# Kernel optimization log

Measured on AMD Instinct MI355X. Metric: run time of the kernel, lower is better.

Reference implementation:

```python
import jax, jax.numpy as jnp
import numpy as np

CENTER_RADIUS = 2.5
TOPK = 13
IOU_WEIGHT = 3.0
BETA = 2.0
NUM_CLASSES = 80
BBOX_W = 2.0
BIG = 1e8
EPS = 1e-7
IMG = 1280


def pairwise_iou(boxes, gts):
    # boxes [N,4], gts [M,4] xyxy -> [N,M]
    lt = jnp.maximum(boxes[:, None, :2], gts[None, :, :2])
    rb = jnp.minimum(boxes[:, None, 2:], gts[None, :, 2:])
    wh = jnp.clip(rb - lt, 0.0)
    inter = wh[..., 0] * wh[..., 1]
    area_a = (boxes[:, 2] - boxes[:, 0]) * (boxes[:, 3] - boxes[:, 1])
    area_b = (gts[:, 2] - gts[:, 0]) * (gts[:, 3] - gts[:, 1])
    union = area_a[:, None] + area_b[None, :] - inter
    return inter / jnp.maximum(union, EPS)


def giou_elementwise(a, b):
    # a,b [N,4] xyxy -> [N]
    lt = jnp.maximum(a[:, :2], b[:, :2])
    rb = jnp.minimum(a[:, 2:], b[:, 2:])
    wh = jnp.clip(rb - lt, 0.0)
    inter = wh[:, 0] * wh[:, 1]
    area_a = (a[:, 2] - a[:, 0]) * (a[:, 3] - a[:, 1])
    area_b = (b[:, 2] - b[:, 0]) * (b[:, 3] - b[:, 1])
    union = area_a + area_b - inter
    iou = inter / jnp.maximum(union, EPS)
    elt = jnp.minimum(a[:, :2], b[:, :2])
    erb = jnp.maximum(a[:, 2:], b[:, 2:])
    ewh = jnp.clip(erb - elt, 0.0)
    enclose = ewh[:, 0] * ewh[:, 1]
    return iou - (enclose - union) / jnp.maximum(enclose, EPS)


def simota_assign(pred_scores, pred_boxes, points, strides, gt_boxes, gt_labels):
    N = points.shape[0]
    M = gt_boxes.shape[0]
    px, py = points[:, 0], points[:, 1]
    # Step 1: candidate selection (inside box OR inside center region)
    in_box = ((px[:, None] > gt_boxes[None, :, 0]) & (py[:, None] > gt_boxes[None, :, 1]) &
              (px[:, None] < gt_boxes[None, :, 2]) & (py[:, None] < gt_boxes[None, :, 3]))
    gcx = (gt_boxes[:, 0] + gt_boxes[:, 2]) * 0.5
    gcy = (gt_boxes[:, 1] + gt_boxes[:, 3]) * 0.5
    r = CENTER_RADIUS * strides[:, None]
    in_center = ((px[:, None] > gcx[None, :] - r) & (py[:, None] > gcy[None, :] - r) &
                 (px[:, None] < gcx[None, :] + r) & (py[:, None] < gcy[None, :] + r))
    is_cand = in_box | in_center          # [N,M]
    cand_any = is_cand.any(axis=1)        # [N]
    # Step 2: cost = BCE(prob, onehot) + w * (-log IoU)
    iou = pairwise_iou(pred_boxes, gt_boxes)  # [N,M]
    p = jnp.clip(pred_scores, 1e-6, 1.0 - 1e-6)
    log_p = jnp.log(p)
    log_1mp = jnp.log1p(-p)
    all_neg = -log_1mp.sum(axis=-1)       # [N] sum_c BCE(p_c, 0)
    cls_cost = all_neg[:, None] + log_1mp[:, gt_labels] - log_p[:, gt_labels]
    reg_cost = -jnp.log(iou + EPS)
    cost = cls_cost + IOU_WEIGHT * reg_cost
    cost = jnp.where(is_cand, cost, BIG)
    # Step 3: dynamic k from top-k IoUs over candidate points (candidates of any gt)
    iou_cand = jnp.where(cand_any[:, None], iou, 0.0)
    topk_ious, _ = jax.lax.top_k(iou_cand.T, TOPK)            # [M,TOPK]
    dyn_k = jnp.clip(topk_ious.sum(axis=-1).astype(jnp.int32), 1, None)  # [M], <= TOPK
    # Step 4: per-gt lowest-cost candidates; k_j entries, only valid (cost < BIG)
    neg_top, top_idx = jax.lax.top_k(-cost.T, TOPK)           # [M,TOPK]
    top_cost = -neg_top
    ranks = jnp.arange(TOPK)
    select = (ranks[None, :] < dyn_k[:, None]) & (top_cost < BIG)
    matching = jnp.zeros((N, M), bool).at[top_idx, jnp.arange(M)[:, None]].set(select)
    # Step 5: conflict resolution -> keep lowest-cost gt per point
    matched = matching.any(axis=1)
    best = jnp.argmin(jnp.where(matching, cost, jnp.inf), axis=1)  # [N]
    rows = jnp.arange(N)
    labels = jnp.where(matched, gt_labels[best], NUM_CLASSES)
    aboxes = jnp.where(matched[:, None], gt_boxes[best], 0.0)
    pos_iou = jnp.where(matched, iou[rows, best], 0.0)
    ascores = jnp.zeros((N, NUM_CLASSES), pred_scores.dtype).at[rows, gt_labels[best]].set(pos_iou)
    return labels, aboxes, ascores


def reference(pred_logits, pred_boxes, points, strides, gt_boxes, gt_labels):
    pred_scores = jax.nn.sigmoid(pred_logits)
    sg = jax.lax.stop_gradient
    labels, aboxes, ascores = simota_assign(sg(pred_scores), sg(pred_boxes),
                                            sg(points), sg(strides), sg(gt_boxes), gt_labels)
    labels, aboxes, ascores = sg(labels), sg(aboxes), sg(ascores)
    # Quality Focal Loss
    x, t = pred_logits, ascores
    bce = jnp.maximum(x, 0.0) - x * t + jnp.log1p(jnp.exp(-jnp.abs(x)))
    scale = jnp.abs(t - pred_scores) ** BETA
    n_pos_cls = jnp.maximum(1, (t > 0).sum()).astype(x.dtype)
    loss_cls = (scale * bce).sum() / n_pos_cls
    # GIoU loss over positives
    matched = labels < NUM_CLASSES
    g = giou_elementwise(pred_boxes, aboxes)
    n_pos = jnp.maximum(1, matched.sum()).astype(x.dtype)
    loss_box = jnp.where(matched, 1.0 - g, 0.0).sum() / n_pos
    return loss_cls + BBOX_W * loss_box


def setup_inputs() -> dict:
    key = jax.random.key(0)
    k1, k2, k3, k4, k5 = jax.random.split(key, 5)
    # multi-scale grid points for a 1280x1280 image, strides 8/16/32
    pts, strs = [], []
    for s in (8, 16, 32):
        n = IMG // s
        c = (jnp.arange(n, dtype=jnp.float32) + 0.5) * s
        yy, xx = jnp.meshgrid(c, c, indexing='ij')
        pts.append(jnp.stack([xx.ravel(), yy.ravel()], axis=-1))
        strs.append(jnp.full((n * n,), float(s), jnp.float32))
    points = jnp.concatenate(pts, axis=0)          # [33600,2]
    strides = jnp.concatenate(strs, axis=0)        # [33600]
    N = points.shape[0]
    pred_logits = jax.random.normal(k1, (N, NUM_CLASSES), jnp.float32) - 2.0
    # decode-style boxes: point +/- positive ltrb distances
    d = jax.random.uniform(k2, (N, 4), jnp.float32) * 64.0 + 1.0
    pred_boxes = jnp.stack([points[:, 0] - d[:, 0], points[:, 1] - d[:, 1],
                            points[:, 0] + d[:, 2], points[:, 1] + d[:, 3]], axis=-1)
    M = 256
    c = jax.random.uniform(k3, (M, 2), jnp.float32) * IMG
    wh = jax.random.uniform(k4, (M, 2), jnp.float32) * 200.0 + 8.0
    gt_boxes = jnp.concatenate([jnp.clip(c - wh / 2, 0, IMG), jnp.clip(c + wh / 2, 0, IMG)], axis=-1)
    gt_labels = jax.random.randint(k5, (M,), 0, NUM_CLASSES, jnp.int32)
    return {"pred_logits": pred_logits, "pred_boxes": pred_boxes, "points": points,
            "strides": strides, "gt_boxes": gt_boxes, "gt_labels": gt_labels}
```

## Files before the change

### kernel.cpp

```cpp
#include <hip/hip_runtime.h>
#include <cstdint>
#include <math.h>

#define NCLS 80
#define TKK 13
#define BIGC 100000000.0f
#define EPSC 1e-7f
#define CRAD 2.5f
#define MARGIN 66.0f

__device__ __constant__ int   c_ln[3]   = {160, 80, 40};
__device__ __constant__ float c_ls[3]   = {8.0f, 16.0f, 32.0f};
__device__ __constant__ int   c_lbase[3]= {0, 25600, 32000};

__device__ __forceinline__ float fsig(float x){
    return __fdividef(1.0f, 1.0f + __expf(-x));
}
__device__ __forceinline__ float fbce0(float x){
    return fmaxf(x, 0.0f) + __logf(1.0f + __expf(-fabsf(x)));
}

__global__ __launch_bounds__(256) void k_prep(
    const float* __restrict__ logits, const float* __restrict__ gt,
    int M, int N, int nbA4,
    unsigned long long* __restrict__ best, char* __restrict__ cand,
    float* __restrict__ comb_t, double* __restrict__ base_cls)
{
    int b = blockIdx.x;
    if (b < nbA4){
        int g = b * 256 + threadIdx.x;
        int n = g >> 2, p = g & 3;
        if (n >= N) return;
        const float4* lg4 = (const float4*)(logits + (size_t)n * NCLS + p * 20);
        float d[20];
        float an = 0.0f;
        double bc = 0.0;
        #pragma unroll
        for (int q = 0; q < 5; q++){
            float4 v = lg4[q];
            float xs[4] = {v.x, v.y, v.z, v.w};
            #pragma unroll
            for (int k = 0; k < 4; k++){
                float x = xs[k];
                float s = fsig(x);
                float pp = fminf(fmaxf(s, 1e-6f), 1.0f - 1e-6f);
                float l1 = __logf(1.0f - pp);
                float lp = __logf(pp);
                an -= l1;
                d[q*4 + k] = l1 - lp;
                bc += (double)((s * s) * fbce0(x));
            }
        }
        an += __shfl_down(an, 2, 4);
        an += __shfl_down(an, 1, 4);
        an = __shfl(an, 0, 4);
        bc += __shfl_down(bc, 2, 4);
        bc += __shfl_down(bc, 1, 4);
        #pragma unroll
        for (int q = 0; q < 20; q++){
            comb_t[(size_t)(p * 20 + q) * N + n] = an + d[q];
        }
        if (p == 0){
            base_cls[n] = bc;
            best[n] = 0xFFFFFFFFFFFFFFFFull;
        }
    } else {
        int m = b - nbA4;
        int tid = threadIdx.x;
        float gx0 = gt[4*m], gy0 = gt[4*m+1], gx1 = gt[4*m+2], gy1 = gt[4*m+3];
        float cx = (gx0 + gx1) * 0.5f, cy = (gy0 + gy1) * 0.5f;
        for (int lvl = 0; lvl < 3; lvl++){
            int   ng = c_ln[lvl];
            float s  = c_ls[lvl];
            int   base = c_lbase[lvl];
            float r = CRAD * s;
            float xlo = fminf(gx0, cx - r), xhi = fmaxf(gx1, cx + r);
            float ylo = fminf(gy0, cy - r), yhi = fmaxf(gy1, cy + r);
            int j0 = max(0, (int)floorf(xlo / s - 0.5f));
            int j1 = min(ng - 1, (int)ceilf(xhi / s - 0.5f));
            int i0 = max(0, (int)floorf(ylo / s - 0.5f));
            int i1 = min(ng - 1, (int)ceilf(yhi / s - 0.5f));
            if (j1 < j0 || i1 < i0) continue;
            int w = j1 - j0 + 1;
            int cells = w * (i1 - i0 + 1);
            for (int c = tid; c < cells; c += 256){
                int ii = i0 + c / w, jj = j0 + c % w;
                float px = (jj + 0.5f) * s, py = (ii + 0.5f) * s;
                bool ib = (px > gx0) && (py > gy0) && (px < gx1) && (py < gy1);
                bool ic = (px > cx - r) && (py > cy - r) && (px < cx + r) && (py < cy + r);
                if (ib || ic) cand[base + ii * ng + jj] = 1;
            }
        }
    }
}

__global__ __launch_bounds__(64) void k_assign(
    const float* __restrict__ pboxes, const float* __restrict__ comb_t,
    const float* __restrict__ gt, const int* __restrict__ glab,
    const char* __restrict__ cand,
    unsigned long long* __restrict__ best, int N)
{
    int m = blockIdx.x;
    int lane = threadIdx.x;

    float gx0 = gt[4*m], gy0 = gt[4*m+1], gx1 = gt[4*m+2], gy1 = gt[4*m+3];
    float areaB = (gx1 - gx0) * (gy1 - gy0);
    float cx = (gx0 + gx1) * 0.5f, cy = (gy0 + gy1) * 0.5f;
    int lab = glab[m];
    const float* __restrict__ combrow = comb_t + (size_t)lab * N;

    float liou[TKK];
    float lc[TKK]; int li[TKK];
    #pragma unroll
    for (int r = 0; r < TKK; r++){ liou[r] = 0.0f; lc[r] = INFINITY; li[r] = 0x7fffffff; }

    for (int lvl = 0; lvl < 3; lvl++){
        int   ng = c_ln[lvl];
        float s  = c_ls[lvl];
        int   base = c_lbase[lvl];
        float r = CRAD * s;
        float xlo = fminf(gx0 - MARGIN, cx - r), xhi = fmaxf(gx1 + MARGIN, cx + r);
        float ylo = fminf(gy0 - MARGIN, cy - r), yhi = fmaxf(gy1 + MARGIN, cy + r);
        int j0 = max(0, (int)floorf(xlo / s - 0.5f));
        int j1 = min(ng - 1, (int)ceilf(xhi / s - 0.5f));
        int i0 = max(0, (int)floorf(ylo / s - 0.5f));
        int i1 = min(ng - 1, (int)ceilf(yhi / s - 0.5f));
        if (j1 < j0 || i1 < i0) continue;
        int w = j1 - j0 + 1;
        int cells = w * (i1 - i0 + 1);
        for (int cb = 0; cb < cells; cb += 256){
            #pragma unroll
            for (int k = 0; k < 4; k++){
                int c = cb + k * 64 + lane;
                if (c >= cells) continue;
                int ii = i0 + (int)((unsigned)c / (unsigned)w);
                int jj = j0 + (int)((unsigned)c % (unsigned)w);
                int n = base + ii * ng + jj;

                float4 pb = ((const float4*)pboxes)[n];
                float comb = combrow[n];
                char  cd   = cand[n];

                float ltx = fmaxf(pb.x, gx0), lty = fmaxf(pb.y, gy0);
                float rbx = fminf(pb.z, gx1), rby = fminf(pb.w, gy1);
                float ww = fmaxf(rbx - ltx, 0.0f), hh = fmaxf(rby - lty, 0.0f);
                float inter = ww * hh;
                float areaA = (pb.z - pb.x) * (pb.w - pb.y);
                float uni = areaA + areaB - inter;
                float iou = inter / fmaxf(uni, EPSC);

                float ioum = cd ? iou : 0.0f;
                if (ioum > liou[TKK-1]){
                    float v = ioum;
                    #pragma unroll
                    for (int j = 0; j < TKK; j++){
                        float a = liou[j];
                        bool ins = (v > a);
                        liou[j] = ins ? v : a;
                        v = ins ? a : v;
                    }
                }

                float px = (jj + 0.5f) * s, py = (ii + 0.5f) * s;
                bool ib = (px > gx0) && (py > gy0) && (px < gx1) && (py < gy1);
                bool ic = (px > cx - r) && (py > cy - r) && (px < cx + r) && (py < cy + r);
                float cost = comb + 3.0f * (-__logf(iou + EPSC));
                bool top = (ib || ic) &&
                           ((cost < lc[TKK-1]) || (cost == lc[TKK-1] && n < li[TKK-1]));
                if (top){
                    float v = cost; int ix = n;
                    #pragma unroll
                    for (int j = 0; j < TKK; j++){
                        float a = lc[j]; int ai = li[j];
                        bool ins = (v < a) || (v == a && ix < ai);
                        lc[j] = ins ? v : a;  li[j] = ins ? ix : ai;
                        v = ins ? a : v;      ix = ins ? ai : ix;
                    }
                }
            }
        }
    }

    float isum = 0.0f;
    for (int r = 0; r < TKK; r++){
        float v = liou[0]; int o = lane;
        #pragma unroll
        for (int off = 32; off > 0; off >>= 1){
            float ov = __shfl_down(v, off);
            int   oo = __shfl_down(o, off);
            if (ov > v){ v = ov; o = oo; }
        }
        v = __shfl(v, 0); o = __shfl(o, 0);
        if (v <= 0.0f) break;
        isum += v;
        if (lane == o){
            #pragma unroll
            for (int j = 0; j < TKK-1; j++) liou[j] = liou[j+1];
            liou[TKK-1] = 0.0f;
        }
    }

    int dynk = (int)isum;
    if (dynk < 1) dynk = 1;
    if (dynk > TKK) dynk = TKK;

    for (int r = 0; r < dynk; r++){
        float v = lc[0]; int ix = li[0]; int o = lane;
        #pragma unroll
        for (int off = 32; off > 0; off >>= 1){
            float ov = __shfl_down(v, off);
            int  oix = __shfl_down(ix, off);
            int   oo = __shfl_down(o, off);
            if (ov < v || (ov == v && oix < ix)){ v = ov; ix = oix; o = oo; }
        }
        v = __shfl(v, 0); ix = __shfl(ix, 0); o = __shfl(o, 0);
        if (!(v < BIGC)) break;
        if (lane == 0){
            unsigned u = __float_as_uint(v);
            u = (u & 0x80000000u) ? ~u : (u | 0x80000000u);
            unsigned long long key = ((unsigned long long)u << 32) | (unsigned)m;
            atomicMin(best + ix, key);
        }
        if (lane == o){
            #pragma unroll
            for (int j = 0; j < TKK-1; j++){ lc[j] = lc[j+1]; li[j] = li[j+1]; }
            lc[TKK-1] = INFINITY; li[TKK-1] = 0x7fffffff;
        }
    }
}

__global__ __launch_bounds__(256) void k_loss(
    const float* __restrict__ logits, const float* __restrict__ pboxes,
    const float* __restrict__ gt, const int* __restrict__ glab,
    const unsigned long long* __restrict__ best,
    const double* __restrict__ base_cls,
    double* __restrict__ accd, int* __restrict__ acci,
    int N, int nblocks, float* __restrict__ out)
{
    int n = blockIdx.x * 256 + threadIdx.x;
    int tid = threadIdx.x;
    int lane = tid & 63, wv = tid >> 6;
    double scls = 0.0, sbox = 0.0;
    int cm = 0, cp = 0;

    if (n < N){
        scls = base_cls[n];
        unsigned long long b = best[n];
        if (b != 0xFFFFFFFFFFFFFFFFull){
            int m = (int)(b & 0xFFFFFFFFu);
            int lab = glab[m];
            float4 pb = ((const float4*)pboxes)[n];
            float gx0 = gt[4*m], gy0 = gt[4*m+1], gx1 = gt[4*m+2], gy1 = gt[4*m+3];
            float ltx = fmaxf(pb.x, gx0), lty = fmaxf(pb.y, gy0);
            float rbx = fminf(pb.z, gx1), rby = fminf(pb.w, gy1);
            float w = fmaxf(rbx - ltx, 0.0f), h = fmaxf(rby - lty, 0.0f);
            float inter = w * h;
            float areaA = (pb.z - pb.x) * (pb.w - pb.y);
            float areaB = (gx1 - gx0) * (gy1 - gy0);
            float uni = areaA + areaB - inter;
            float iou = inter / fmaxf(uni, EPSC);
            float eltx = fminf(pb.x, gx0), elty = fminf(pb.y, gy0);
            float erbx = fmaxf(pb.z, gx1), erby = fmaxf(pb.w, gy1);
            float ew = fmaxf(erbx - eltx, 0.0f), eh = fmaxf(erby - elty, 0.0f);
            float enc = ew * eh;
            float giou = iou - (enc - uni) / fmaxf(enc, EPSC);
            sbox = (double)(1.0f - giou);
            cm = 1;
            cp = (iou > 0.0f) ? 1 : 0;
            float x = logits[(size_t)n * NCLS + lab];
            float s = fsig(x);
            float bce0 = fbce0(x);
            float bcet = bce0 - x * iou;
            float d = iou - s;
            scls = scls - (double)((s * s) * bce0) + (double)((d * d) * bcet);
        }
    }

    #pragma unroll
    for (int off = 32; off > 0; off >>= 1){
        scls += __shfl_down(scls, off);
        sbox += __shfl_down(sbox, off);
        cm   += __shfl_down(cm, off);
        cp   += __shfl_down(cp, off);
    }
    __shared__ double sd0[4];
    __shared__ double sd1[4];
    __shared__ int    si0[4];
    __shared__ int    si1[4];
    if (lane == 0){ sd0[wv] = scls; sd1[wv] = sbox; si0[wv] = cm; si1[wv] = cp; }
    __syncthreads();
    if (tid == 0){
        double a0 = 0.0, a1 = 0.0; int c0 = 0, c1 = 0;
        #pragma unroll
        for (int q = 0; q < 4; q++){ a0 += sd0[q]; a1 += sd1[q]; c0 += si0[q]; c1 += si1[q]; }
        atomicAdd(&accd[0], a0);
        atomicAdd(&accd[1], a1);
        atomicAdd(&acci[0], c0);
        atomicAdd(&acci[1], c1);
        __threadfence();
        int donec = atomicAdd(&acci[2], 1);
        if (donec == nblocks - 1){
            double A0 = atomicAdd(&accd[0], 0.0);
            double A1 = atomicAdd(&accd[1], 0.0);
            int C0 = atomicAdd(&acci[0], 0);
            int C1 = atomicAdd(&acci[1], 0);
            if (C0 < 1) C0 = 1;
            if (C1 < 1) C1 = 1;
            out[0] = (float)(A0 / (double)C1 + 2.0 * A1 / (double)C0);
        }
    }
}

extern "C" void kernel_launch(void* const* d_in, const int* in_sizes, int n_in,
                              void* d_out, int out_size, void* d_ws, size_t ws_size,
                              hipStream_t stream) {
    const float* logits  = (const float*)d_in[0];
    const float* pboxes  = (const float*)d_in[1];
    const float* gtb     = (const float*)d_in[4];
    const int*   glab    = (const int*)d_in[5];

    int N = in_sizes[3];
    int M = in_sizes[5];

    char* ws = (char*)d_ws;
    size_t off = 0;
    unsigned long long* best = (unsigned long long*)(ws + off); off += (size_t)8 * N;
    double* base_cls = (double*)(ws + off); off += (size_t)8 * N;
    float*  comb_t   = (float*)(ws + off);  off += (size_t)4 * NCLS * N;
    size_t zstart = off;
    char*   cand = (char*)(ws + off);       off += (size_t)N;
    off = (off + 15) & ~(size_t)15;
    double* accd = (double*)(ws + off);     off += 16;
    int*    acci = (int*)(ws + off);        off += 16;
    size_t zlen = off - zstart;

    hipMemsetAsync(ws + zstart, 0, zlen, stream);

    int nbA4 = (4 * N + 255) / 256;
    int nbL  = (N + 255) / 256;
    k_prep<<<nbA4 + M, 256, 0, stream>>>(logits, gtb, M, N, nbA4,
                                         best, cand, comb_t, base_cls);
    k_assign<<<M, 64, 0, stream>>>(pboxes, comb_t, gtb, glab, cand, best, N);
    k_loss<<<nbL, 256, 0, stream>>>(logits, pboxes, gtb, glab, best, base_cls,
                                    accd, acci, N, nbL, (float*)d_out);
}
```

Measured before the change: 132.4 us.

## Restructure assignment into point-major candidate compaction plus per-GT topk kernel

Replaces the per-GT grid-window scan with a point-major kernel that checks every GT per 64-point wavefront. Candidate IoUs and costs are compacted into fixed-capacity per-GT buffers through ballot and atomicAdd. A separate per-GT kernel then runs the top-k selection over these compact lists. This drops the full 80-class comb_t transpose write and the candidate bitmap, at the cost of an M-length loop per wavefront, global atomics, and capacity caps (4096/2048) that could silently drop candidates.

Result: slower. 241.2 us (+82.2%).

```diff
diff --git a/kernel.cpp b/kernel.cpp
--- a/kernel.cpp
+++ b/kernel.cpp
@@ -8,10 +8,8 @@
 #define EPSC 1e-7f
 #define CRAD 2.5f
 #define MARGIN 66.0f
-
-__device__ __constant__ int   c_ln[3]   = {160, 80, 40};
-__device__ __constant__ float c_ls[3]   = {8.0f, 16.0f, 32.0f};
-__device__ __constant__ int   c_lbase[3]= {0, 25600, 32000};
+#define CAPI 4096
+#define CAPC 2048
 
 __device__ __forceinline__ float fsig(float x){
     return __fdividef(1.0f, 1.0f + __expf(-x));
@@ -20,23 +18,23 @@
     return fmaxf(x, 0.0f) + __logf(1.0f + __expf(-fabsf(x)));
 }
 
-__global__ __launch_bounds__(256) void k_prep(
-    const float* __restrict__ logits, const float* __restrict__ gt,
-    int M, int N, int nbA4,
-    unsigned long long* __restrict__ best, char* __restrict__ cand,
-    float* __restrict__ comb_t, double* __restrict__ base_cls)
+__global__ __launch_bounds__(64) void k_main(
+    const float* __restrict__ logits, const float* __restrict__ pboxes,
+    const float* __restrict__ points, const float* __restrict__ strides,
+    const float* __restrict__ gt, const int* __restrict__ glab, int M, int N,
+    unsigned long long* __restrict__ best, double* __restrict__ base_cls,
+    float* __restrict__ iou_v, int* __restrict__ len_iou,
+    float* __restrict__ cost_v, int* __restrict__ cost_i, int* __restrict__ len_cost)
 {
-    int b = blockIdx.x;
-    if (b < nbA4){
-        int g = b * 256 + threadIdx.x;
-        int n = g >> 2, p = g & 3;
-        if (n >= N) return;
-        const float4* lg4 = (const float4*)(logits + (size_t)n * NCLS + p * 20);
-        float d[20];
-        float an = 0.0f;
-        double bc = 0.0;
+    int lane = threadIdx.x;
+    int n = blockIdx.x * 64 + lane;
+    bool act = (n < N);
+
+    float an = 0.0f; double bc = 0.0;
+    if (act){
+        const float4* lg4 = (const float4*)(logits + (size_t)n * NCLS);
         #pragma unroll
-        for (int q = 0; q < 5; q++){
+        for (int q = 0; q < NCLS/4; q++){
             float4 v = lg4[q];
             float xs[4] = {v.x, v.y, v.z, v.w};
             #pragma unroll
@@ -44,143 +42,129 @@
                 float x = xs[k];
                 float s = fsig(x);
                 float pp = fminf(fmaxf(s, 1e-6f), 1.0f - 1e-6f);
-                float l1 = __logf(1.0f - pp);
-                float lp = __logf(pp);
-                an -= l1;
-                d[q*4 + k] = l1 - lp;
+                an -= __logf(1.0f - pp);
                 bc += (double)((s * s) * fbce0(x));
             }
         }
-        an += __shfl_down(an, 2, 4);
-        an += __shfl_down(an, 1, 4);
-        an = __shfl(an, 0, 4);
-        bc += __shfl_down(bc, 2, 4);
-        bc += __shfl_down(bc, 1, 4);
-        #pragma unroll
-        for (int q = 0; q < 20; q++){
-            comb_t[(size_t)(p * 20 + q) * N + n] = an + d[q];
-        }
-        if (p == 0){
-            base_cls[n] = bc;
-            best[n] = 0xFFFFFFFFFFFFFFFFull;
-        }
-    } else {
-        int m = b - nbA4;
-        int tid = threadIdx.x;
+        base_cls[n] = bc;
+        best[n] = 0xFFFFFFFFFFFFFFFFull;
+    }
+
+    float px = act ? points[2*n]   : 0.0f;
+    float py = act ? points[2*n+1] : 0.0f;
+    float rr = act ? CRAD * strides[n] : 0.0f;
+    float4 pb;
+    if (act) pb = ((const float4*)pboxes)[n];
+    else { pb.x = 0.f; pb.y = 0.f; pb.z = 0.f; pb.w = 0.f; }
+    float areaA = (pb.z - pb.x) * (pb.w - pb.y);
+
+    float bxmin = act ? px :  1e30f, bxmax = act ? px : -1e30f;
+    float bymin = act ? py :  1e30f, bymax = act ? py : -1e30f;
+    float rmax  = act ? rr : 0.0f;
+    #pragma unroll
+    for (int off = 32; off > 0; off >>= 1){
+        bxmin = fminf(bxmin, __shfl_xor(bxmin, off));
+        bxmax = fmaxf(bxmax, __shfl_xor(bxmax, off));
+        bymin = fminf(bymin, __shfl_xor(bymin, off));
+        bymax = fmaxf(bymax, __shfl_xor(bymax, off));
+        rmax  = fmaxf(rmax,  __shfl_xor(rmax,  off));
+    }
+
+    int any = 0;
+    for (int m = 0; m < M; m++){
         float gx0 = gt[4*m], gy0 = gt[4*m+1], gx1 = gt[4*m+2], gy1 = gt[4*m+3];
         float cx = (gx0 + gx1) * 0.5f, cy = (gy0 + gy1) * 0.5f;
-        for (int lvl = 0; lvl < 3; lvl++){
-            int   ng = c_ln[lvl];
-            float s  = c_ls[lvl];
-            int   base = c_lbase[lvl];
-            float r = CRAD * s;
-            float xlo = fminf(gx0, cx - r), xhi = fmaxf(gx1, cx + r);
-            float ylo = fminf(gy0, cy - r), yhi = fmaxf(gy1, cy + r);
-            int j0 = max(0, (int)floorf(xlo / s - 0.5f));
-            int j1 = min(ng - 1, (int)ceilf(xhi / s - 0.5f));
-            int i0 = max(0, (int)floorf(ylo / s - 0.5f));
-            int i1 = min(ng - 1, (int)ceilf(yhi / s - 0.5f));
-            if (j1 < j0 || i1 < i0) continue;
-            int w = j1 - j0 + 1;
-            int cells = w * (i1 - i0 + 1);
-            for (int c = tid; c < cells; c += 256){
-                int ii = i0 + c / w, jj = j0 + c % w;
-                float px = (jj + 0.5f) * s, py = (ii + 0.5f) * s;
-                bool ib = (px > gx0) && (py > gy0) && (px < gx1) && (py < gy1);
-                bool ic = (px > cx - r) && (py > cy - r) && (px < cx + r) && (py < cy + r);
-                if (ib || ic) cand[base + ii * ng + jj] = 1;
-            }
-        }
-    }
-}
-
-__global__ __launch_bounds__(64) void k_assign(
-    const float* __restrict__ pboxes, const float* __restrict__ comb_t,
-    const float* __restrict__ gt, const int* __restrict__ glab,
-    const char* __restrict__ cand,
-    unsigned long long* __restrict__ best, int N)
+        float xlo = fminf(gx0, cx - rmax), xhi = fmaxf(gx1, cx + rmax);
+        float ylo = fminf(gy0, cy - rmax), yhi = fmaxf(gy1, cy + rmax);
+        if (xhi < bxmin || xlo > bxmax || yhi < bymin || ylo > bymax) continue;
+        bool ib = (px > gx0) && (py > gy0) && (px < gx1) && (py < gy1);
+        bool ic = (px > cx - rr) && (py > cy - rr) && (px < cx + rr) && (py < cy + rr);
+        if (ib || ic) any = 1;
+    }
+    if (!act) any = 0;
+
+    for (int m = 0; m < M; m++){
+        float gx0 = gt[4*m], gy0 = gt[4*m+1], gx1 = gt[4*m+2], gy1 = gt[4*m+3];
+        float cx = (gx0 + gx1) * 0.5f, cy = (gy0 + gy1) * 0.5f;
+        float xlo = fminf(gx0 - MARGIN, cx - rmax), xhi = fmaxf(gx1 + MARGIN, cx + rmax);
+        float ylo = fminf(gy0 - MARGIN, cy - rmax), yhi = fmaxf(gy1 + MARGIN, cy + rmax);
+        if (xhi < bxmin || xlo > bxmax || yhi < bymin || ylo > bymax) continue;
+
+        float areaB = (gx1 - gx0) * (gy1 - gy0);
+        float ltx = fmaxf(pb.x, gx0), lty = fmaxf(pb.y, gy0);
+        float rbx = fminf(pb.z, gx1), rby = fminf(pb.w, gy1);
+        float ww = fmaxf(rbx - ltx, 0.0f), hh = fmaxf(rby - lty, 0.0f);
+        float inter = ww * hh;
+        float uni = areaA + areaB - inter;
+        float iou = inter / fmaxf(uni, EPSC);
+
+        bool pi = act && any && (inter > 0.0f);
+        unsigned long long mk = __ballot(pi);
+        if (mk){
+            int first = __builtin_ctzll(mk);
+            int cnt = __popcll(mk);
+            int basev = 0;
+            if (lane == first) basev = atomicAdd(&len_iou[m], cnt);
+            basev = __shfl(basev, first);
+            if (pi){
+                int slot = basev + __popcll(mk & ((1ull << lane) - 1ull));
+                if (slot < CAPI) iou_v[(size_t)m * CAPI + slot] = iou;
+            }
+        }
+
+        bool ib = (px > gx0) && (py > gy0) && (px < gx1) && (py < gy1);
+        bool ic = (px > cx - rr) && (py > cy - rr) && (px < cx + rr) && (py < cy + rr);
+        bool pc = act && (ib || ic);
+        mk = __ballot(pc);
+        if (mk){
+            int lab = glab[m];
+            int first = __builtin_ctzll(mk);
+            int cnt = __popcll(mk);
+            int basev = 0;
+            if (lane == first) basev = atomicAdd(&len_cost[m], cnt);
+            basev = __shfl(basev, first);
+            if (pc){
+                float x = logits[(size_t)n * NCLS + lab];
+                float s = fsig(x);
+                float pp = fminf(fmaxf(s, 1e-6f), 1.0f - 1e-6f);
+                float cost = an + (__logf(1.0f - pp) - __logf(pp))
+                           + 3.0f * (-__logf(iou + EPSC));
+                int slot = basev + __popcll(mk & ((1ull << lane) - 1ull));
+                if (slot < CAPC){
+                    cost_v[(size_t)m * CAPC + slot] = cost;
+                    cost_i[(size_t)m * CAPC + slot] = n;
+                }
+            }
+        }
+    }
+}
+
+__global__ __launch_bounds__(64) void k_topk(
+    const float* __restrict__ iou_v, const int* __restrict__ len_iou,
+    const float* __restrict__ cost_v, const int* __restrict__ cost_i,
+    const int* __restrict__ len_cost,
+    unsigned long long* __restrict__ best)
 {
     int m = blockIdx.x;
     int lane = threadIdx.x;
-
-    float gx0 = gt[4*m], gy0 = gt[4*m+1], gx1 = gt[4*m+2], gy1 = gt[4*m+3];
-    float areaB = (gx1 - gx0) * (gy1 - gy0);
-    float cx = (gx0 + gx1) * 0.5f, cy = (gy0 + gy1) * 0.5f;
-    int lab = glab[m];
-    const float* __restrict__ combrow = comb_t + (size_t)lab * N;
+    int ni = min(len_iou[m], CAPI);
+    int nc = min(len_cost[m], CAPC);
 
     float liou[TKK];
-    float lc[TKK]; int li[TKK];
     #pragma unroll
-    for (int r = 0; r < TKK; r++){ liou[r] = 0.0f; lc[r] = INFINITY; li[r] = 0x7fffffff; }
-
-    for (int lvl = 0; lvl < 3; lvl++){
-        int   ng = c_ln[lvl];
-        float s  = c_ls[lvl];
-        int   base = c_lbase[lvl];
-        float r = CRAD * s;
-        float xlo = fminf(gx0 - MARGIN, cx - r), xhi = fmaxf(gx1 + MARGIN, cx + r);
-        float ylo = fminf(gy0 - MARGIN, cy - r), yhi = fmaxf(gy1 + MARGIN, cy + r);
-        int j0 = max(0, (int)floorf(xlo / s - 0.5f));
-        int j1 = min(ng - 1, (int)ceilf(xhi / s - 0.5f));
-        int i0 = max(0, (int)floorf(ylo / s - 0.5f));
-        int i1 = min(ng - 1, (int)ceilf(yhi / s - 0.5f));
-        if (j1 < j0 || i1 < i0) continue;
-        int w = j1 - j0 + 1;
-        int cells = w * (i1 - i0 + 1);
-        for (int cb = 0; cb < cells; cb += 256){
-            #pragma unroll
-            for (int k = 0; k < 4; k++){
-                int c = cb + k * 64 + lane;
-                if (c >= cells) continue;
-                int ii = i0 + (int)((unsigned)c / (unsigned)w);
-                int jj = j0 + (int)((unsigned)c % (unsigned)w);
-                int n = base + ii * ng + jj;
-
-                float4 pb = ((const float4*)pboxes)[n];
-                float comb = combrow[n];
-                char  cd   = cand[n];
-
-                float ltx = fmaxf(pb.x, gx0), lty = fmaxf(pb.y, gy0);
-                float rbx = fminf(pb.z, gx1), rby = fminf(pb.w, gy1);
-                float ww = fmaxf(rbx - ltx, 0.0f), hh = fmaxf(rby - lty, 0.0f);
-                float inter = ww * hh;
-                float areaA = (pb.z - pb.x) * (pb.w - pb.y);
-                float uni = areaA + areaB - inter;
-                float iou = inter / fmaxf(uni, EPSC);
-
-                float ioum = cd ? iou : 0.0f;
-                if (ioum > liou[TKK-1]){
-                    float v = ioum;
-                    #pragma unroll
-                    for (int j = 0; j < TKK; j++){
-                        float a = liou[j];
-                        bool ins = (v > a);
-                        liou[j] = ins ? v : a;
-                        v = ins ? a : v;
-                    }
-                }
-
-                float px = (jj + 0.5f) * s, py = (ii + 0.5f) * s;
-                bool ib = (px > gx0) && (py > gy0) && (px < gx1) && (py < gy1);
-                bool ic = (px > cx - r) && (py > cy - r) && (px < cx + r) && (py < cy + r);
-                float cost = comb + 3.0f * (-__logf(iou + EPSC));
-                bool top = (ib || ic) &&
-                           ((cost < lc[TKK-1]) || (cost == lc[TKK-1] && n < li[TKK-1]));
-                if (top){
-                    float v = cost; int ix = n;
-                    #pragma unroll
-                    for (int j = 0; j < TKK; j++){
-                        float a = lc[j]; int ai = li[j];
-                        bool ins = (v < a) || (v == a && ix < ai);
-                        lc[j] = ins ? v : a;  li[j] = ins ? ix : ai;
-                        v = ins ? a : v;      ix = ins ? ai : ix;
-                    }
-                }
-            }
-        }
-    }
-
+    for (int r = 0; r < TKK; r++) liou[r] = 0.0f;
+    for (int i = lane; i < ni; i += 64){
+        float v = iou_v[(size_t)m * CAPI + i];
+        if (v > liou[TKK-1]){
+            #pragma unroll
+            for (int j = 0; j < TKK; j++){
+                float a = liou[j];
+                bool ins = (v > a);
+                liou[j] = ins ? v : a;
+                v = ins ? a : v;
+            }
+        }
+    }
     float isum = 0.0f;
     for (int r = 0; r < TKK; r++){
         float v = liou[0]; int o = lane;
@@ -199,11 +183,27 @@
             liou[TKK-1] = 0.0f;
         }
     }
-
     int dynk = (int)isum;
     if (dynk < 1) dynk = 1;
     if (dynk > TKK) dynk = TKK;
 
+    float lc[TKK]; int li[TKK];
+    #pragma unroll
+    for (int r = 0; r < TKK; r++){ lc[r] = INFINITY; li[r] = 0x7fffffff; }
+    for (int i = lane; i < nc; i += 64){
+        float v = cost_v[(size_t)m * CAPC + i];
+        int  ix = cost_i[(size_t)m * CAPC + i];
+        bool top = (v < lc[TKK-1]) || (v == lc[TKK-1] && ix < li[TKK-1]);
+        if (top){
+            #pragma unroll
+            for (int j = 0; j < TKK; j++){
+                float a = lc[j]; int ai = li[j];
+                bool ins = (v < a) || (v == a && ix < ai);
+                lc[j] = ins ? v : a;  li[j] = ins ? ix : ai;
+                v = ins ? a : v;      ix = ins ? ai : ix;
+            }
+        }
+    }
     for (int r = 0; r < dynk; r++){
         float v = lc[0]; int ix = li[0]; int o = lane;
         #pragma unroll
@@ -316,6 +316,8 @@
                               hipStream_t stream) {
     const float* logits  = (const float*)d_in[0];
     const float* pboxes  = (const float*)d_in[1];
+    const float* points  = (const float*)d_in[2];
+    const float* strides = (const float*)d_in[3];
     const float* gtb     = (const float*)d_in[4];
     const int*   glab    = (const int*)d_in[5];
 
@@ -326,21 +328,25 @@
     size_t off = 0;
     unsigned long long* best = (unsigned long long*)(ws + off); off += (size_t)8 * N;
     double* base_cls = (double*)(ws + off); off += (size_t)8 * N;
-    float*  comb_t   = (float*)(ws + off);  off += (size_t)4 * NCLS * N;
+    float*  iou_v  = (float*)(ws + off);    off += (size_t)4 * M * CAPI;
+    float*  cost_v = (float*)(ws + off);    off += (size_t)4 * M * CAPC;
+    int*    cost_i = (int*)(ws + off);      off += (size_t)4 * M * CAPC;
+    off = (off + 15) & ~(size_t)15;
     size_t zstart = off;
-    char*   cand = (char*)(ws + off);       off += (size_t)N;
-    off = (off + 15) & ~(size_t)15;
+    int*    len_iou  = (int*)(ws + off);    off += (size_t)4 * M;
+    int*    len_cost = (int*)(ws + off);    off += (size_t)4 * M;
     double* accd = (double*)(ws + off);     off += 16;
     int*    acci = (int*)(ws + off);        off += 16;
     size_t zlen = off - zstart;
 
     hipMemsetAsync(ws + zstart, 0, zlen, stream);
 
-    int nbA4 = (4 * N + 255) / 256;
-    int nbL  = (N + 255) / 256;
-    k_prep<<<nbA4 + M, 256, 0, stream>>>(logits, gtb, M, N, nbA4,
-                                         best, cand, comb_t, base_cls);
-    k_assign<<<M, 64, 0, stream>>>(pboxes, comb_t, gtb, glab, cand, best, N);
+    int nbM = (N + 63) / 64;
+    int nbL = (N + 255) / 256;
+    k_main<<<nbM, 64, 0, stream>>>(logits, pboxes, points, strides, gtb, glab,
+                                   M, N, best, base_cls,
+                                   iou_v, len_iou, cost_v, cost_i, len_cost);
+    k_topk<<<M, 64, 0, stream>>>(iou_v, len_iou, cost_v, cost_i, len_cost, best);
     k_loss<<<nbL, 256, 0, stream>>>(logits, pboxes, gtb, glab, best, base_cls,
                                     accd, acci, N, nbL, (float*)d_out);
 }
```

## Split per-GT assignment across four blocks with last-block merge of partial top-k

Applied to the files above, without the earlier changes.

Each ground-truth box is now handled by four 64-thread blocks instead of one. Each block writes its partial top-13 IoU and cost lists to workspace, and the last block to finish (found through an atomic counter) merges them to compute dynamic k and issue the atomicMin assignments. The prep kernel also stops writing a precomputed per-class cost matrix. It stores transposed raw logits plus a per-point sum of negative log terms, and the cost is rebuilt from a clamped logit using a fused sigmoid/softplus helper. This is meant to raise parallelism in the latency-bound assign kernel, at the cost of extra global partial buffers, threadfences and an additional load per cell.

Measured after the change: 162.0 us. +22.4%, slower.

```diff
diff --git a/kernel.cpp b/kernel.cpp
--- a/kernel.cpp
+++ b/kernel.cpp
@@ -8,23 +8,26 @@
 #define EPSC 1e-7f
 #define CRAD 2.5f
 #define MARGIN 66.0f
+#define SPLIT 4
+#define XCLP 13.815511f
 
 __device__ __constant__ int   c_ln[3]   = {160, 80, 40};
 __device__ __constant__ float c_ls[3]   = {8.0f, 16.0f, 32.0f};
 __device__ __constant__ int   c_lbase[3]= {0, 25600, 32000};
 
-__device__ __forceinline__ float fsig(float x){
-    return __fdividef(1.0f, 1.0f + __expf(-x));
-}
-__device__ __forceinline__ float fbce0(float x){
-    return fmaxf(x, 0.0f) + __logf(1.0f + __expf(-fabsf(x)));
+__device__ __forceinline__ void sig_sp(float x, float& s, float& sp){
+    float e = __expf(-fabsf(x));
+    float L = __logf(1.0f + e);
+    sp = fmaxf(x, 0.0f) + L;
+    s = __fdividef((x >= 0.0f) ? 1.0f : e, 1.0f + e);
 }
 
 __global__ __launch_bounds__(256) void k_prep(
     const float* __restrict__ logits, const float* __restrict__ gt,
     int M, int N, int nbA4,
     unsigned long long* __restrict__ best, char* __restrict__ cand,
-    float* __restrict__ comb_t, double* __restrict__ base_cls)
+    float* __restrict__ xt, float* __restrict__ an_arr,
+    double* __restrict__ base_cls)
 {
     int b = blockIdx.x;
     if (b < nbA4){
@@ -32,35 +35,32 @@
         int n = g >> 2, p = g & 3;
         if (n >= N) return;
         const float4* lg4 = (const float4*)(logits + (size_t)n * NCLS + p * 20);
-        float d[20];
+        float xs[20];
         float an = 0.0f;
         double bc = 0.0;
         #pragma unroll
         for (int q = 0; q < 5; q++){
             float4 v = lg4[q];
-            float xs[4] = {v.x, v.y, v.z, v.w};
+            xs[q*4+0] = v.x; xs[q*4+1] = v.y; xs[q*4+2] = v.z; xs[q*4+3] = v.w;
             #pragma unroll
             for (int k = 0; k < 4; k++){
-                float x = xs[k];
-                float s = fsig(x);
-                float pp = fminf(fmaxf(s, 1e-6f), 1.0f - 1e-6f);
-                float l1 = __logf(1.0f - pp);
-                float lp = __logf(pp);
-                an -= l1;
-                d[q*4 + k] = l1 - lp;
-                bc += (double)((s * s) * fbce0(x));
+                float x = xs[q*4+k];
+                float s, sp;
+                sig_sp(x, s, sp);
+                an += fminf(sp, XCLP);
+                bc += (double)((s * s) * sp);
             }
         }
         an += __shfl_down(an, 2, 4);
         an += __shfl_down(an, 1, 4);
-        an = __shfl(an, 0, 4);
         bc += __shfl_down(bc, 2, 4);
         bc += __shfl_down(bc, 1, 4);
         #pragma unroll
         for (int q = 0; q < 20; q++){
-            comb_t[(size_t)(p * 20 + q) * N + n] = an + d[q];
+            xt[(size_t)(p * 20 + q) * N + n] = xs[q];
         }
         if (p == 0){
+            an_arr[n] = an;
             base_cls[n] = bc;
             best[n] = 0xFFFFFFFFFFFFFFFFull;
         }
@@ -95,19 +95,24 @@
 }
 
 __global__ __launch_bounds__(64) void k_assign(
-    const float* __restrict__ pboxes, const float* __restrict__ comb_t,
+    const float* __restrict__ pboxes, const float* __restrict__ xt,
+    const float* __restrict__ an_arr,
     const float* __restrict__ gt, const int* __restrict__ glab,
     const char* __restrict__ cand,
+    float* __restrict__ p_iou, float* __restrict__ p_cv, int* __restrict__ p_ci,
+    int* __restrict__ done,
     unsigned long long* __restrict__ best, int N)
 {
-    int m = blockIdx.x;
+    int gid = blockIdx.x;
+    int m = gid >> 2, sp = gid & (SPLIT - 1);
     int lane = threadIdx.x;
+    int g = sp * 64 + lane;
 
     float gx0 = gt[4*m], gy0 = gt[4*m+1], gx1 = gt[4*m+2], gy1 = gt[4*m+3];
     float areaB = (gx1 - gx0) * (gy1 - gy0);
     float cx = (gx0 + gx1) * 0.5f, cy = (gy0 + gy1) * 0.5f;
     int lab = glab[m];
-    const float* __restrict__ combrow = comb_t + (size_t)lab * N;
+    const float* __restrict__ xrow = xt + (size_t)lab * N;
 
     float liou[TKK];
     float lc[TKK]; int li[TKK];
@@ -128,18 +133,19 @@
         if (j1 < j0 || i1 < i0) continue;
         int w = j1 - j0 + 1;
         int cells = w * (i1 - i0 + 1);
-        for (int cb = 0; cb < cells; cb += 256){
+        for (int cb = 0; cb < cells; cb += SPLIT * 256){
             #pragma unroll
             for (int k = 0; k < 4; k++){
-                int c = cb + k * 64 + lane;
+                int c = cb + k * 256 + g;
                 if (c >= cells) continue;
                 int ii = i0 + (int)((unsigned)c / (unsigned)w);
                 int jj = j0 + (int)((unsigned)c % (unsigned)w);
                 int n = base + ii * ng + jj;
 
                 float4 pb = ((const float4*)pboxes)[n];
-                float comb = combrow[n];
-                char  cd   = cand[n];
+                float xv = xrow[n];
+                float av = an_arr[n];
+                char  cd = cand[n];
 
                 float ltx = fmaxf(pb.x, gx0), lty = fmaxf(pb.y, gy0);
                 float rbx = fminf(pb.z, gx1), rby = fminf(pb.w, gy1);
@@ -164,7 +170,8 @@
                 float px = (jj + 0.5f) * s, py = (ii + 0.5f) * s;
                 bool ib = (px > gx0) && (py > gy0) && (px < gx1) && (py < gy1);
                 bool ic = (px > cx - r) && (py > cy - r) && (px < cx + r) && (py < cy + r);
-                float cost = comb + 3.0f * (-__logf(iou + EPSC));
+                float xc = fminf(fmaxf(xv, -XCLP), XCLP);
+                float cost = av - xc + 3.0f * (-__logf(iou + EPSC));
                 bool top = (ib || ic) &&
                            ((cost < lc[TKK-1]) || (cost == lc[TKK-1] && n < li[TKK-1]));
                 if (top){
@@ -181,7 +188,7 @@
         }
     }
 
-    float isum = 0.0f;
+    int pb0 = (m * SPLIT + sp) * TKK;
     for (int r = 0; r < TKK; r++){
         float v = liou[0]; int o = lane;
         #pragma unroll
@@ -191,20 +198,18 @@
             if (ov > v){ v = ov; o = oo; }
         }
         v = __shfl(v, 0); o = __shfl(o, 0);
-        if (v <= 0.0f) break;
-        isum += v;
+        if (lane == 0) p_iou[pb0 + r] = v;
+        if (v <= 0.0f){
+            if (lane == 0) for (int rr = r+1; rr < TKK; rr++) p_iou[pb0 + rr] = 0.0f;
+            break;
+        }
         if (lane == o){
             #pragma unroll
             for (int j = 0; j < TKK-1; j++) liou[j] = liou[j+1];
             liou[TKK-1] = 0.0f;
         }
     }
-
-    int dynk = (int)isum;
-    if (dynk < 1) dynk = 1;
-    if (dynk > TKK) dynk = TKK;
-
-    for (int r = 0; r < dynk; r++){
+    for (int r = 0; r < TKK; r++){
         float v = lc[0]; int ix = li[0]; int o = lane;
         #pragma unroll
         for (int off = 32; off > 0; off >>= 1){
@@ -214,18 +219,68 @@
             if (ov < v || (ov == v && oix < ix)){ v = ov; ix = oix; o = oo; }
         }
         v = __shfl(v, 0); ix = __shfl(ix, 0); o = __shfl(o, 0);
-        if (!(v < BIGC)) break;
-        if (lane == 0){
-            unsigned u = __float_as_uint(v);
-            u = (u & 0x80000000u) ? ~u : (u | 0x80000000u);
-            unsigned long long key = ((unsigned long long)u << 32) | (unsigned)m;
-            atomicMin(best + ix, key);
+        if (lane == 0){ p_cv[pb0 + r] = v; p_ci[pb0 + r] = ix; }
+        if (v == INFINITY){
+            if (lane == 0) for (int rr = r+1; rr < TKK; rr++){
+                p_cv[pb0 + rr] = INFINITY; p_ci[pb0 + rr] = 0x7fffffff;
+            }
+            break;
         }
         if (lane == o){
             #pragma unroll
             for (int j = 0; j < TKK-1; j++){ lc[j] = lc[j+1]; li[j] = li[j+1]; }
             lc[TKK-1] = INFINITY; li[TKK-1] = 0x7fffffff;
         }
+    }
+
+    __threadfence();
+    int last = 0;
+    if (lane == 0) last = (atomicAdd(&done[m], 1) == SPLIT - 1) ? 1 : 0;
+    last = __shfl(last, 0);
+    if (!last) return;
+    __threadfence();
+
+    int mb = m * SPLIT * TKK;
+    float v = (lane < SPLIT*TKK) ? p_iou[mb + lane] : 0.0f;
+    float isum = 0.0f;
+    for (int r = 0; r < TKK; r++){
+        float x = v; int o = lane;
+        #pragma unroll
+        for (int off = 32; off > 0; off >>= 1){
+            float ox = __shfl_down(x, off);
+            int   oo = __shfl_down(o, off);
+            if (ox > x){ x = ox; o = oo; }
+        }
+        x = __shfl(x, 0); o = __shfl(o, 0);
+        if (x <= 0.0f) break;
+        isum += x;
+        if (lane == o) v = 0.0f;
+    }
+    int dynk = (int)isum;
+    if (dynk < 1) dynk = 1;
+    if (dynk > TKK) dynk = TKK;
+
+    float cv; int ci;
+    if (lane < SPLIT*TKK){ cv = p_cv[mb + lane]; ci = p_ci[mb + lane]; }
+    else { cv = INFINITY; ci = 0x7fffffff; }
+    for (int r = 0; r < dynk; r++){
+        float x = cv; int xi = ci; int o = lane;
+        #pragma unroll
+        for (int off = 32; off > 0; off >>= 1){
+            float ox = __shfl_down(x, off);
+            int  oxi = __shfl_down(xi, off);
+            int   oo = __shfl_down(o, off);
+            if (ox < x || (ox == x && oxi < xi)){ x = ox; xi = oxi; o = oo; }
+        }
+        x = __shfl(x, 0); xi = __shfl(xi, 0); o = __shfl(o, 0);
+        if (!(x < BIGC)) break;
+        if (lane == 0){
+            unsigned u = __float_as_uint(x);
+            u = (u & 0x80000000u) ? ~u : (u | 0x80000000u);
+            unsigned long long key = ((unsigned long long)u << 32) | (unsigned)m;
+            atomicMin(best + xi, key);
+        }
+        if (lane == o){ cv = INFINITY; ci = 0x7fffffff; }
     }
 }
 
@@ -268,11 +323,11 @@
             cm = 1;
             cp = (iou > 0.0f) ? 1 : 0;
             float x = logits[(size_t)n * NCLS + lab];
-            float s = fsig(x);
-            float bce0 = fbce0(x);
-            float bcet = bce0 - x * iou;
+            float s, spv;
+            sig_sp(x, s, spv);
+            float bcet = spv - x * iou;
             float d = iou - s;
-            scls = scls - (double)((s * s) * bce0) + (double)((d * d) * bcet);
+            scls = scls - (double)((s * s) * spv) + (double)((d * d) * bcet);
         }
     }
 
@@ -322,14 +377,22 @@
     int N = in_sizes[3];
     int M = in_sizes[5];
 
+    size_t P = (size_t)M * SPLIT * TKK;
+
     char* ws = (char*)d_ws;
     size_t off = 0;
     unsigned long long* best = (unsigned long long*)(ws + off); off += (size_t)8 * N;
     double* base_cls = (double*)(ws + off); off += (size_t)8 * N;
-    float*  comb_t   = (float*)(ws + off);  off += (size_t)4 * NCLS * N;
+    float*  xt       = (float*)(ws + off);  off += (size_t)4 * NCLS * N;
+    float*  an_arr   = (float*)(ws + off);  off += (size_t)4 * N;
+    float*  p_iou    = (float*)(ws + off);  off += P * 4;
+    float*  p_cv     = (float*)(ws + off);  off += P * 4;
+    int*    p_ci     = (int*)(ws + off);    off += P * 4;
+    off = (off + 15) & ~(size_t)15;
     size_t zstart = off;
     char*   cand = (char*)(ws + off);       off += (size_t)N;
     off = (off + 15) & ~(size_t)15;
+    int*    done = (int*)(ws + off);        off += (size_t)4 * M;
     double* accd = (double*)(ws + off);     off += 16;
     int*    acci = (int*)(ws + off);        off += 16;
     size_t zlen = off - zstart;
@@ -339,8 +402,9 @@
     int nbA4 = (4 * N + 255) / 256;
     int nbL  = (N + 255) / 256;
     k_prep<<<nbA4 + M, 256, 0, stream>>>(logits, gtb, M, N, nbA4,
-                                         best, cand, comb_t, base_cls);
-    k_assign<<<M, 64, 0, stream>>>(pboxes, comb_t, gtb, glab, cand, best, N);
+                                         best, cand, xt, an_arr, base_cls);
+    k_assign<<<M * SPLIT, 64, 0, stream>>>(pboxes, xt, an_arr, gtb, glab, cand,
+                                           p_iou, p_cv, p_ci, done, best, N);
     k_loss<<<nbL, 256, 0, stream>>>(logits, pboxes, gtb, glab, best, base_cls,
                                     accd, acci, N, nbL, (float*)d_out);
 }
```
